# Kernel optimization log

Hardware: AMD Instinct MI355X
Metric: run time of the kernel (lower is better)

Reference implementation:

```python
import jax, jax.numpy as jnp
import numpy as np

B, L, D_OUT, D_HIDDEN = 16, 4096, 1024, 512
MAX_PHASE = 6.28
R_MIN, R_MAX = 0.9, 0.999


def setup_inputs() -> dict:
    key = jax.random.key(0)
    ks = jax.random.split(key, 8)
    x = jax.random.normal(ks[0], (B, L, D_OUT), dtype=jnp.float32)
    # theta_init: log(max_phase * u)
    u_th = jax.random.uniform(ks[1], (D_HIDDEN,), dtype=jnp.float32)
    theta_log = jnp.log(MAX_PHASE * u_th)
    # nu_init: log(-0.5 * log(u * (r_max^2 - r_min^2) + r_min^2))
    u_nu = jax.random.uniform(ks[2], (D_HIDDEN,), dtype=jnp.float32)
    nu_log = jnp.log(-0.5 * jnp.log(u_nu * (R_MAX**2 - R_MIN**2) + R_MIN**2))
    # gamma_log_init from (nu_log, theta_log)
    diag_lambda = jnp.exp(-jnp.exp(nu_log) + 1j * jnp.exp(theta_log))
    gamma_log = jnp.log(jnp.sqrt(1.0 - jnp.abs(diag_lambda) ** 2))
    b_norm = jnp.sqrt(2.0 * D_OUT)
    c_norm = jnp.sqrt(float(D_HIDDEN))
    B_re = jax.random.normal(ks[3], (D_HIDDEN, D_OUT), dtype=jnp.float32) / b_norm
    B_im = jax.random.normal(ks[4], (D_HIDDEN, D_OUT), dtype=jnp.float32) / b_norm
    C_re = jax.random.normal(ks[5], (D_OUT, D_HIDDEN), dtype=jnp.float32) / c_norm
    C_im = jax.random.normal(ks[6], (D_OUT, D_HIDDEN), dtype=jnp.float32) / c_norm
    D = jax.random.normal(ks[7], (D_OUT,), dtype=jnp.float32)
    return {"x": x, "theta_log": theta_log, "nu_log": nu_log, "gamma_log": gamma_log,
            "B_re": B_re, "B_im": B_im, "C_re": C_re, "C_im": C_im, "D": D}


def _binop(q_i, q_j):
    # associative op for linear recurrence h_t = A_t * h_{t-1} + b_t (diagonal A)
    A_i, b_i = q_i
    A_j, b_j = q_j
    return (A_j * A_i, A_j * b_i + b_j)


def reference(x, theta_log, nu_log, gamma_log, B_re, B_im, C_re, C_im, D):
    diag_lambda = jnp.exp(-jnp.exp(nu_log) + 1j * jnp.exp(theta_log))  # (H,)
    B_norm = (B_re + 1j * B_im) * jnp.exp(gamma_log)[:, None]          # (H, D)
    C = C_re + 1j * C_im                                               # (D, H)
    # input projection: Bu_t = B_norm @ x_t -> (B, L, H) complex
    Bu = jnp.einsum('hd,bld->blh', B_norm, x.astype(B_norm.dtype))
    Lam = jnp.broadcast_to(diag_lambda, Bu.shape)
    # parallel scan over the sequence axis
    _, h = jax.lax.associative_scan(_binop, (Lam, Bu), axis=1)         # (B, L, H)
    # readout: y_t = Re[C h_t] + D * x_t
    y = jnp.einsum('oh,blh->blo', C, h).real + D * x
    return (y, h[:, -1])
```

## Files before the change

### kernel.cpp

```cpp
#include <hip/hip_runtime.h>

#define NB 16
#define NL 4096
#define NDO 1024
#define NH 512
#define NM (NB*NL)
#define NK 1024
#define NN 1024
#define CH 128
#define NCHUNK (NL/CH)
#define YCOUNT ((size_t)NM*NDO)
#define HCOUNT ((size_t)NB*NH)

typedef unsigned short u16;
typedef float f32x4 __attribute__((ext_vector_type(4)));
typedef unsigned int u32x4 __attribute__((ext_vector_type(4)));
typedef __bf16 bf16x8 __attribute__((ext_vector_type(8)));

__device__ __forceinline__ u16 f2bf(float f){
  unsigned u = __float_as_uint(f);
  unsigned r = u + 0x7fffu + ((u >> 16) & 1u);
  return (u16)(r >> 16);
}
__device__ __forceinline__ float bf2f(u16 v){ return __uint_as_float(((unsigned)v) << 16); }
__device__ __forceinline__ unsigned pack2(float a, float b){
  return (unsigned)f2bf(a) | ((unsigned)f2bf(b) << 16);
}

__device__ __forceinline__ void gld_lds16(const u16* g, u16* l){
  __builtin_amdgcn_global_load_lds(
      (const __attribute__((address_space(1))) unsigned int*)g,
      (__attribute__((address_space(3))) unsigned int*)l,
      16, 0, 0);
}


__global__ void prep_w1(const float* __restrict__ Bre, const float* __restrict__ Bim,
                        const float* __restrict__ gl, u16* __restrict__ W1){
  int i = blockIdx.x * blockDim.x + threadIdx.x;
  if (i >= NH * NDO) return;
  int h = i / NDO, d = i % NDO;
  float g = expf(gl[h]);
  W1[(size_t)h * NK + d]        = f2bf(Bre[i] * g);
  W1[(size_t)(NH + h) * NK + d] = f2bf(Bim[i] * g);
}

__global__ void prep_w2(const float* __restrict__ Cre, const float* __restrict__ Cim,
                        u16* __restrict__ W2){
  int i = blockIdx.x * blockDim.x + threadIdx.x;
  if (i >= NDO * NH) return;
  int o = i / NH, k = i % NH;
  W2[(size_t)o * NK + k]      = f2bf(Cre[i]);
  W2[(size_t)o * NK + NH + k] = f2bf(-Cim[i]);
}

__global__ void prep_lam(const float* __restrict__ theta_log, const float* __restrict__ nu_log,
                         float* __restrict__ lam){
  int h = threadIdx.x;
  if (h >= NH) return;
  float nu = expf(nu_log[h]);
  float th = expf(theta_log[h]);
  float mag = expf(-nu);
  float lre = mag * cosf(th), lim = mag * sinf(th);
  double pre = (double)lre, pim = (double)lim;
  #pragma unroll
  for (int s = 0; s < 7; s++){
    double nr = pre*pre - pim*pim;
    double ni = 2.0*pre*pim;
    pre = nr; pim = ni;
  }
  lam[h]        = lre;
  lam[NH + h]   = lim;
  lam[2*NH + h] = (float)pre;
  lam[3*NH + h] = (float)pim;
}

__global__ __launch_bounds__(256) void convert_x(const float* __restrict__ X, u16* __restrict__ Xb){
  size_t i = ((size_t)blockIdx.x * 256 + threadIdx.x) * 8;
  f32x4 a = *(const f32x4*)(X + i);
  f32x4 b = *(const f32x4*)(X + i + 4);
  u32x4 p;
  p[0] = pack2(a[0], a[1]); p[1] = pack2(a[2], a[3]);
  p[2] = pack2(b[0], b[1]); p[3] = pack2(b[2], b[3]);
  *(u32x4*)(Xb + i) = p;
}

template<int MODE>
__global__ __launch_bounds__(256) void gemm_pipe(const u16* __restrict__ A,
                                                 const u16* __restrict__ W,
                                                 const float* __restrict__ Xf,
                                                 const u16* __restrict__ Xh,
                                                 const float* __restrict__ Dv,
                                                 u16* __restrict__ outB,
                                                 float* __restrict__ outF){
  __shared__ __align__(16) u16 A0[128][32];
  __shared__ __align__(16) u16 B0[128][32];
  __shared__ __align__(16) u16 A1[128][32];
  __shared__ __align__(16) u16 B1[128][32];
  const int tid = threadIdx.x;
  const int bid = blockIdx.x;
  const int lid = (bid & 7) * 512 + (bid >> 3);
  const int m0 = (lid >> 3) << 7;
  const int n0 = (lid & 7) << 7;
  const int w = tid >> 6, lane = tid & 63;
  const int wm = w >> 1, wn = w & 1;

  const int sr = lane >> 2;
  const int sc = (lane & 3) << 3;
  const u16* ag = A + (size_t)(m0 + w*32 + sr) * NK + sc;
  const u16* bg = W + (size_t)(n0 + w*32 + sr) * NK + sc;

  f32x4 acc[4][4];
#pragma unroll
  for (int i = 0; i < 4; i++)
#pragma unroll
    for (int j = 0; j < 4; j++) acc[i][j] = (f32x4){0.f,0.f,0.f,0.f};

  const int klane = (lane >> 4) << 3;
  const int rowa = wm*64 + (lane & 15);
  const int rowb = wn*64 + (lane & 15);

#define STAGE0(k0) do {                               \
    gld_lds16(ag + (k0),          &A0[w*32][0]);      \
    gld_lds16(ag + (k0) + 16*NK,  &A0[w*32+16][0]);   \
    gld_lds16(bg + (k0),          &B0[w*32][0]);      \
    gld_lds16(bg + (k0) + 16*NK,  &B0[w*32+16][0]);   \
  } while(0)
#define STAGE1(k0) do {                               \
    gld_lds16(ag + (k0),          &A1[w*32][0]);      \
    gld_lds16(ag + (k0) + 16*NK,  &A1[w*32+16][0]);   \
    gld_lds16(bg + (k0),          &B1[w*32][0]);      \
    gld_lds16(bg + (k0) + 16*NK,  &B1[w*32+16][0]);   \
  } while(0)
#define COMPUTE(AT, BT) do {                                        \
    bf16x8 af[4], bv[4];                                            \
    _Pragma("unroll")                                               \
    for (int i = 0; i < 4; i++){                                    \
      af[i] = *(const bf16x8*)&AT[rowa + i*16][klane];              \
      bv[i] = *(const bf16x8*)&BT[rowb + i*16][klane];              \
    }                                                               \
    _Pragma("unroll")                                               \
    for (int i = 0; i < 4; i++)                                     \
      _Pragma("unroll")                                             \
      for (int j = 0; j < 4; j++)                                   \
        acc[i][j] = __builtin_amdgcn_mfma_f32_16x16x32_bf16(af[i], bv[j], acc[i][j], 0, 0, 0); \
  } while(0)
#define WAITVM(n) asm volatile("s_waitcnt vmcnt(" #n ")" ::: "memory")
#define LGKM0()   asm volatile("s_waitcnt lgkmcnt(0)" ::: "memory")
#define BAR()     asm volatile("s_barrier" ::: "memory")

  STAGE0(0);
  STAGE1(32);
  WAITVM(4);
  BAR();

  for (int k0 = 0; k0 < NK - 64; k0 += 64) {
    COMPUTE(A0, B0);
    LGKM0();
    BAR();
    STAGE0(k0 + 64);
    WAITVM(4);
    BAR();
    COMPUTE(A1, B1);
    LGKM0();
    BAR();
    STAGE1(k0 + 96);
    WAITVM(4);
    BAR();
  }
  COMPUTE(A0, B0);
  LGKM0();
  WAITVM(0);
  BAR();
  COMPUTE(A1, B1);

#undef STAGE0
#undef STAGE1
#undef COMPUTE
#undef WAITVM
#undef LGKM0
#undef BAR

  const int r0 = (lane >> 4) << 2;
  const int col = lane & 15;
#pragma unroll
  for (int i = 0; i < 4; i++){
    int gm = m0 + wm*64 + i*16 + r0;
#pragma unroll
    for (int j = 0; j < 4; j++){
      int gn = n0 + wn*64 + j*16 + col;
      if constexpr (MODE == 0) {
#pragma unroll
        for (int r = 0; r < 4; r++)
          outB[(size_t)(gm + r) * NN + gn] = f2bf(acc[i][j][r]);
      } else if constexpr (MODE == 1) {
        float dv = Dv[gn];
#pragma unroll
        for (int r = 0; r < 4; r++){
          size_t oidx = (size_t)(gm + r) * NDO + gn;
          outF[oidx] = acc[i][j][r] + dv * Xf[oidx];
        }
      } else {
        float dv = Dv[gn];
#pragma unroll
        for (int r = 0; r < 4; r++){
          size_t oidx = (size_t)(gm + r) * NDO + gn;
          outF[oidx] = acc[i][j][r] + dv * bf2f(Xh[oidx]);
        }
      }
    }
  }
}


__global__ __launch_bounds__(256) void gemm1_legacy(const float* __restrict__ X,
                                                    const u16* __restrict__ W1,
                                                    u16* __restrict__ Bu){
  __shared__ __align__(16) u16 Alds[128][32];
  __shared__ __align__(16) u16 Blds[128][32];
  const int tid = threadIdx.x;
  const int bid = blockIdx.x;
  const int lid = (bid & 7) * 512 + (bid >> 3);
  const int m0 = (lid >> 3) << 7;
  const int n0 = (lid & 7) << 7;
  const int w = tid >> 6, lane = tid & 63;
  const int wm = w >> 1, wn = w & 1;
  f32x4 acc[4][4];
#pragma unroll
  for (int i = 0; i < 4; i++)
#pragma unroll
    for (int j = 0; j < 4; j++) acc[i][j] = (f32x4){0.f,0.f,0.f,0.f};

  const int srow = tid >> 1;
  const int skseg = (tid & 1) << 4;
  const float* xp = X + (size_t)(m0 + srow) * NK + skseg;
  const u16*  wp  = W1 + (size_t)(n0 + srow) * NK + skseg;

  const int klane = (lane >> 4) << 3;
  const int rowa = wm*64 + (lane & 15);
  const int rowb = wn*64 + (lane & 15);

  for (int k0 = 0; k0 < NK; k0 += 32) {
    __syncthreads();
    f32x4 v0 = *(const f32x4*)(xp + k0 + 0);
    f32x4 v1 = *(const f32x4*)(xp + k0 + 4);
    f32x4 v2 = *(const f32x4*)(xp + k0 + 8);
    f32x4 v3 = *(const f32x4*)(xp + k0 + 12);
    u32x4 q0 = *(const u32x4*)(wp + k0);
    u32x4 q1 = *(const u32x4*)(wp + k0 + 8);
    u32x4 p0, p1;
    p0[0] = pack2(v0[0], v0[1]); p0[1] = pack2(v0[2], v0[3]);
    p0[2] = pack2(v1[0], v1[1]); p0[3] = pack2(v1[2], v1[3]);
    p1[0] = pack2(v2[0], v2[1]); p1[1] = pack2(v2[2], v2[3]);
    p1[2] = pack2(v3[0], v3[1]); p1[3] = pack2(v3[2], v3[3]);
    *(u32x4*)&Alds[srow][skseg]     = p0;
    *(u32x4*)&Alds[srow][skseg + 8] = p1;
    *(u32x4*)&Blds[srow][skseg]     = q0;
    *(u32x4*)&Blds[srow][skseg + 8] = q1;
    __syncthreads();
    bf16x8 af[4], bv[4];
#pragma unroll
    for (int i = 0; i < 4; i++){
      af[i] = *(const bf16x8*)&Alds[rowa + i*16][klane];
      bv[i] = *(const bf16x8*)&Blds[rowb + i*16][klane];
    }
#pragma unroll
    for (int i = 0; i < 4; i++)
#pragma unroll
      for (int j = 0; j < 4; j++)
        acc[i][j] = __builtin_amdgcn_mfma_f32_16x16x32_bf16(af[i], bv[j], acc[i][j], 0, 0, 0);
  }

  const int r0 = (lane >> 4) << 2;
  const int col = lane & 15;
#pragma unroll
  for (int i = 0; i < 4; i++){
    int gm = m0 + wm*64 + i*16 + r0;
#pragma unroll
    for (int j = 0; j < 4; j++){
      int gn = n0 + wn*64 + j*16 + col;
#pragma unroll
      for (int r = 0; r < 4; r++)
        Bu[(size_t)(gm + r) * NN + gn] = f2bf(acc[i][j][r]);
    }
  }
}


__global__ __launch_bounds__(512) void scan_carry(const u16* __restrict__ Bu,
                                                  const float* __restrict__ lam,
                                                  float* __restrict__ carry){
  const int h = threadIdx.x;
  const int bc = blockIdx.x;
  const int b = bc / NCHUNK, c = bc % NCHUNK;
  const float lre = lam[h], lim = lam[NH + h];
  float hre = 0.f, him = 0.f;
  size_t base = (size_t)(b * NL + c * CH) * NN;
  for (int j = 0; j < CH; j++){
    float bre = bf2f(Bu[base + (size_t)j*NN + h]);
    float bim = bf2f(Bu[base + (size_t)j*NN + NH + h]);
    float nre = lre*hre - lim*him + bre;
    float nim = lre*him + lim*hre + bim;
    hre = nre; him = nim;
  }
  size_t ci = ((size_t)bc * NH + h) * 2;
  carry[ci] = hre; carry[ci + 1] = him;
}

__global__ __launch_bounds__(512) void scan_combine(const float* __restrict__ carry,
                                                    const float* __restrict__ lam,
                                                    float* __restrict__ hstart){
  const int h = threadIdx.x;
  const int b = blockIdx.x;
  const float Pre = lam[2*NH + h], Pim = lam[3*NH + h];
  float are = 0.f, aim = 0.f;
  for (int c = 0; c < NCHUNK; c++){
    size_t idx = ((size_t)(b * NCHUNK + c) * NH + h) * 2;
    hstart[idx] = are; hstart[idx + 1] = aim;
    float cre = carry[idx], cim = carry[idx + 1];
    float nre = Pre*are - Pim*aim + cre;
    float nim = Pre*aim + Pim*are + cim;
    are = nre; aim = nim;
  }
}

__global__ __launch_bounds__(512) void scan_fixup(u16* __restrict__ Bu,
                                                  const float* __restrict__ lam,
                                                  const float* __restrict__ hstart,
                                                  float* __restrict__ out, int out_size){
  const int h = threadIdx.x;
  const int bc = blockIdx.x;
  const int b = bc / NCHUNK, c = bc % NCHUNK;
  const float lre = lam[h], lim = lam[NH + h];
  size_t si = ((size_t)bc * NH + h) * 2;
  const float sre = hstart[si], sim = hstart[si + 1];
  float hre = 0.f, him = 0.f;
  float pre = lre, pim = lim;
  size_t base = (size_t)(b * NL + c * CH) * NN;
  for (int j = 0; j < CH; j++){
    float bre = bf2f(Bu[base + (size_t)j*NN + h]);
    float bim = bf2f(Bu[base + (size_t)j*NN + NH + h]);
    float nre = lre*hre - lim*him + bre;
    float nim = lre*him + lim*hre + bim;
    hre = nre; him = nim;
    float vre = hre + pre*sre - pim*sim;
    float vim = him + pre*sim + pim*sre;
    Bu[base + (size_t)j*NN + h]      = f2bf(vre);
    Bu[base + (size_t)j*NN + NH + h] = f2bf(vim);
    if (c == NCHUNK - 1 && j == CH - 1){
      size_t ore_i = YCOUNT + (size_t)b * NH + h;
      size_t oim_i = YCOUNT + HCOUNT + (size_t)b * NH + h;
      if (ore_i < (size_t)out_size) out[ore_i] = vre;
      if (oim_i < (size_t)out_size) out[oim_i] = vim;
    }
    float qre = pre*lre - pim*lim;
    float qim = pre*lim + pim*lre;
    pre = qre; pim = qim;
  }
}


extern "C" void kernel_launch(void* const* d_in, const int* in_sizes, int n_in,
                              void* d_out, int out_size, void* d_ws, size_t ws_size,
                              hipStream_t stream) {
  const float* x         = (const float*)d_in[0];
  const float* theta_log = (const float*)d_in[1];
  const float* nu_log    = (const float*)d_in[2];
  const float* gamma_log = (const float*)d_in[3];
  const float* Bre       = (const float*)d_in[4];
  const float* Bim       = (const float*)d_in[5];
  const float* Cre       = (const float*)d_in[6];
  const float* Cim       = (const float*)d_in[7];
  const float* Dv        = (const float*)d_in[8];
  float* out = (float*)d_out;
  char* ws = (char*)d_ws;

  u16*   W1     = (u16*)(ws);
  u16*   W2     = (u16*)(ws + (2u << 20));
  float* lam    = (float*)(ws + (4u << 20));
  float* carry  = (float*)(ws + (5u << 20));
  float* hstart = (float*)(ws + (7u << 20));
  u16*   Bu     = (u16*)(ws + (16u << 20));
  u16*   Xb     = (u16*)(ws + (144u << 20));
  size_t need_base = (16u << 20) + (size_t)NM * NN * 2;
  size_t need_fast = need_base + (size_t)NM * NK * 2;
  if (ws_size < need_base) return;
  const bool fast = (ws_size >= need_fast);

  prep_w1<<<(NH * NDO + 255) / 256, 256, 0, stream>>>(Bre, Bim, gamma_log, W1);
  prep_w2<<<(NDO * NH + 255) / 256, 256, 0, stream>>>(Cre, Cim, W2);
  prep_lam<<<1, 512, 0, stream>>>(theta_log, nu_log, lam);

  if (fast) {
    convert_x<<<(int)(YCOUNT / (256*8)), 256, 0, stream>>>(x, Xb);
    gemm_pipe<0><<<4096, 256, 0, stream>>>(Xb, W1, nullptr, nullptr, nullptr, Bu, nullptr);
  } else {
    gemm1_legacy<<<4096, 256, 0, stream>>>(x, W1, Bu);
  }

  scan_carry<<<NB * NCHUNK, 512, 0, stream>>>(Bu, lam, carry);
  scan_combine<<<NB, 512, 0, stream>>>(carry, lam, hstart);
  scan_fixup<<<NB * NCHUNK, 512, 0, stream>>>(Bu, lam, hstart, out, out_size);

  if (fast) {
    gemm_pipe<2><<<4096, 256, 0, stream>>>(Bu, W2, nullptr, Xb, Dv, nullptr, out);
  } else {
    gemm_pipe<1><<<4096, 256, 0, stream>>>(Bu, W2, x, nullptr, Dv, nullptr, out);
  }
}
```

Measured before the change: 598.5 us.

## Add 256x256-tile GEMM kernel with 512 threads for input projection

Introduces a new GEMM kernel using 256x256 output tiles, 64-wide K steps, 8 waves per block, and double-buffered LDS with swizzled direct global-to-LDS loads. It replaces the 128x128 pipelined kernel for the first projection only, aiming to raise arithmetic intensity and cut global/LDS traffic per FLOP. The larger tile uses 128 KB of LDS and many accumulator registers, which limits occupancy, and the grid shrinks to 1024 blocks.

```diff
diff --git a/kernel.cpp b/kernel.cpp
--- a/kernel.cpp
+++ b/kernel.cpp
@@ -83,6 +83,135 @@
   p[0] = pack2(a[0], a[1]); p[1] = pack2(a[2], a[3]);
   p[2] = pack2(b[0], b[1]); p[3] = pack2(b[2], b[3]);
   *(u32x4*)(Xb + i) = p;
+}
+
+
+__device__ __forceinline__ void stage_tile(const u16* Ag, const u16* Bg, int kt,
+                                           u16 (&AB)[256][64], u16 (&BB)[256][64], int w){
+  const u16* a = Ag + (size_t)kt * 64;
+  const u16* b = Bg + (size_t)kt * 64;
+  #pragma unroll
+  for (int s = 0; s < 4; s++){
+    gld_lds16(a + (size_t)s * 8 * NK, &AB[w*32 + s*8][0]);
+    gld_lds16(b + (size_t)s * 8 * NK, &BB[w*32 + s*8][0]);
+  }
+}
+
+__device__ __forceinline__ void compute_tile(const u16 (&AB)[256][64], const u16 (&BB)[256][64],
+                                             f32x4 (&acc)[8][4], int wr, int wc,
+                                             int c15, int sw0, int sw1){
+  #pragma unroll
+  for (int ks = 0; ks < 2; ks++){
+    const int sw = (ks == 0) ? sw0 : sw1;
+    bf16x8 af[8], bv[4];
+    #pragma unroll
+    for (int i = 0; i < 8; i++)
+      af[i] = *(const bf16x8*)(&AB[wr*128 + i*16 + c15][0] + sw);
+    #pragma unroll
+    for (int j = 0; j < 4; j++)
+      bv[j] = *(const bf16x8*)(&BB[wc*64 + j*16 + c15][0] + sw);
+    #pragma unroll
+    for (int i = 0; i < 8; i++)
+      #pragma unroll
+      for (int j = 0; j < 4; j++)
+        acc[i][j] = __builtin_amdgcn_mfma_f32_16x16x32_bf16(af[i], bv[j], acc[i][j], 0, 0, 0);
+  }
+}
+
+template<int MODE>
+__global__ __launch_bounds__(512, 2) void gemm_256(const u16* __restrict__ A,
+                                                   const u16* __restrict__ W,
+                                                   const float* __restrict__ Xf,
+                                                   const u16* __restrict__ Xh,
+                                                   const float* __restrict__ Dv,
+                                                   u16* __restrict__ outB,
+                                                   float* __restrict__ outF){
+  __shared__ __align__(16) u16 A0[256][64];
+  __shared__ __align__(16) u16 B0[256][64];
+  __shared__ __align__(16) u16 A1[256][64];
+  __shared__ __align__(16) u16 B1[256][64];
+  const int tid = threadIdx.x;
+  const int bid = blockIdx.x;
+  const int lid = (bid & 7) * 128 + (bid >> 3);
+  const int m0 = (lid >> 2) << 8;
+  const int n0 = (lid & 3) << 8;
+  const int w = tid >> 6, lane = tid & 63;
+  const int wr = w >> 2, wc = w & 3;
+
+  const int grow = lane >> 3;
+  const int gcol = ((lane & 7) ^ grow) << 3;
+  const u16* Ag = A + (size_t)(m0 + w*32 + grow) * NK + gcol;
+  const u16* Bg = W + (size_t)(n0 + w*32 + grow) * NK + gcol;
+
+  const int c15 = lane & 15;
+  const int qb  = lane >> 4;
+  const int sw0 = ((qb    ) ^ (lane & 7)) << 3;
+  const int sw1 = ((qb | 4) ^ (lane & 7)) << 3;
+
+  f32x4 acc[8][4];
+  #pragma unroll
+  for (int m = 0; m < 8; m++)
+    #pragma unroll
+    for (int n = 0; n < 4; n++) acc[m][n] = (f32x4){0.f,0.f,0.f,0.f};
+
+#define LGKM0() asm volatile("s_waitcnt lgkmcnt(0)" ::: "memory")
+#define VM0()   asm volatile("s_waitcnt vmcnt(0)" ::: "memory")
+#define BAR()   __builtin_amdgcn_s_barrier()
+
+  stage_tile(Ag, Bg, 0, A0, B0, w);
+  VM0();
+  BAR();
+
+  #pragma unroll 1
+  for (int kt = 0; kt < NK/64; kt += 2){
+    stage_tile(Ag, Bg, kt + 1, A1, B1, w);
+    compute_tile(A0, B0, acc, wr, wc, c15, sw0, sw1);
+    LGKM0();
+    BAR();
+    VM0();
+    BAR();
+    if (kt + 2 < NK/64){
+      stage_tile(Ag, Bg, kt + 2, A0, B0, w);
+      compute_tile(A1, B1, acc, wr, wc, c15, sw0, sw1);
+      LGKM0(); BAR();
+      VM0();  BAR();
+    } else {
+      compute_tile(A1, B1, acc, wr, wc, c15, sw0, sw1);
+    }
+  }
+
+#undef LGKM0
+#undef VM0
+#undef BAR
+
+  const int r4 = (lane >> 4) << 2;
+  #pragma unroll
+  for (int m = 0; m < 8; m++){
+    int gm = m0 + wr*128 + m*16 + r4;
+    #pragma unroll
+    for (int n = 0; n < 4; n++){
+      int gn = n0 + wc*64 + n*16 + c15;
+      if constexpr (MODE == 0) {
+        #pragma unroll
+        for (int r = 0; r < 4; r++)
+          outB[(size_t)(gm + r) * NN + gn] = f2bf(acc[m][n][r]);
+      } else if constexpr (MODE == 1) {
+        float dv = Dv[gn];
+        #pragma unroll
+        for (int r = 0; r < 4; r++){
+          size_t oidx = (size_t)(gm + r) * NDO + gn;
+          outF[oidx] = acc[m][n][r] + dv * Xf[oidx];
+        }
+      } else {
+        float dv = Dv[gn];
+        #pragma unroll
+        for (int r = 0; r < 4; r++){
+          size_t oidx = (size_t)(gm + r) * NDO + gn;
+          outF[oidx] = acc[m][n][r] + dv * bf2f(Xh[oidx]);
+        }
+      }
+    }
+  }
 }
 
 template<int MODE>
@@ -391,9 +520,11 @@
   prep_w2<<<(NDO * NH + 255) / 256, 256, 0, stream>>>(Cre, Cim, W2);
   prep_lam<<<1, 512, 0, stream>>>(theta_log, nu_log, lam);
 
+  const int g256 = (NM / 256) * (NN / 256);
+
   if (fast) {
     convert_x<<<(int)(YCOUNT / (256*8)), 256, 0, stream>>>(x, Xb);
-    gemm_pipe<0><<<4096, 256, 0, stream>>>(Xb, W1, nullptr, nullptr, nullptr, Bu, nullptr);
+    gemm_256<0><<<g256, 512, 0, stream>>>(Xb, W1, nullptr, nullptr, nullptr, Bu, nullptr);
   } else {
     gemm1_legacy<<<4096, 256, 0, stream>>>(x, W1, Bu);
   }
```

After: 875.7 us. 46.3% more time.
